# Optimization experiments

Measured on AMD Instinct MI355X. Metric: run time of the kernel, lower is better.

## Reference

```python
import jax, jax.numpy as jnp
import numpy as np

G = 512          # graphs in batch
NPG = 128        # nodes per graph (equal-sized so decoder batches)
TEMP = 0.1       # SimilarityDecoder temperature


def setup_inputs() -> dict:
    key = jax.random.key(0)
    ks = jax.random.split(key, 10)
    N, D, K, H, T = G * NPG, 512, 1024, 128, 10
    return {
        "x": jax.random.normal(ks[0], (N, D), jnp.float32),
        "batch": jnp.repeat(jnp.arange(G, dtype=jnp.int64), NPG),
        "codebook_input": jax.random.normal(ks[1], (K, D), jnp.float32),
        "fc1_w": jax.random.normal(ks[2], (H, D), jnp.float32) * (1.0 / np.sqrt(D)),
        "fc1_b": jax.random.normal(ks[3], (H,), jnp.float32) * 0.01,
        "fc2_w": jax.random.normal(ks[4], (D, H), jnp.float32) * (1.0 / np.sqrt(H)),
        "fc2_b": jax.random.normal(ks[5], (D,), jnp.float32) * 0.01,
        "causal": jax.random.normal(ks[6], (K, K), jnp.float32),
        "cls_w": jax.random.normal(ks[7], (T, D), jnp.float32) * (1.0 / np.sqrt(D)),
        "cls_b": jax.random.normal(ks[8], (T,), jnp.float32) * 0.01,
    }


def _segment_mean(v, batch, num_segments):
    s = jax.ops.segment_sum(v, batch, num_segments=num_segments)
    cnt = jax.ops.segment_sum(jnp.ones((v.shape[0], 1), v.dtype), batch, num_segments=num_segments)
    return s / jnp.maximum(cnt, 1.0)


def _batched_adj(z):
    # SimilarityDecoder: per-graph sigmoid(norm_z @ norm_z.T / temp); graphs equal-sized -> [G, n, n]
    zg = z.reshape(G, NPG, -1)
    zn = zg / jnp.maximum(jnp.linalg.norm(zg, axis=-1, keepdims=True), 1e-12)
    return jax.nn.sigmoid(jnp.einsum("gnd,gmd->gnm", zn, zn) / TEMP)


def reference(x, batch, codebook_input, fc1_w, fc1_b, fc2_w, fc2_b, causal, cls_w, cls_b):
    K = causal.shape[0]
    I = jnp.eye(K, dtype=x.dtype)

    # ---- VectorQuantizer ----
    h = jax.nn.sigmoid(codebook_input @ fc1_w.T + fc1_b)
    codebook_transformed = h @ fc2_w.T + fc2_b                 # [K, D]
    causal_effect = causal * (1.0 - I) + I                     # off-diag causal + identity
    cs = jax.nn.sigmoid(codebook_transformed)
    causal_diag = causal * I
    causal_cb = causal_effect @ (causal_diag @ cs)             # [K, D]
    counter_matrix = causal * (1.0 - I)                        # DegreeLayer assumed: off-diagonal mask
    counter_cb = causal_effect @ (counter_matrix @ cs)         # [K, D]

    # ---- ClassLayer ----
    pooled_x = _segment_mean(x, batch, G)                      # [G, D]
    # squared euclidean distances x vs causal_cb -> argmin codebook index
    d2 = (jnp.sum(x * x, 1, keepdims=True)
          - 2.0 * (x @ causal_cb.T)
          + jnp.sum(causal_cb * causal_cb, 1))                 # [N, K]
    idx = jnp.argmin(d2, axis=1)                               # [N]
    causal_nodes = x + causal_cb[idx]
    counter_nodes = counter_cb[idx]
    z_nodes = codebook_transformed[idx]                        # [N, D]
    pooled_causal = _segment_mean(causal_nodes, batch, G)
    pooled_counter = _segment_mean(counter_nodes, batch, G)
    causal_pre = pooled_causal @ cls_w.T + cls_b
    counter_pre = pooled_counter @ cls_w.T + cls_b
    y_pre = pooled_x @ jax.lax.stop_gradient(cls_w).T + jax.lax.stop_gradient(cls_b)

    # ---- SimilarityDecoder ----
    A_ori = _batched_adj(x)                                    # [G, n, n]
    A_rec = _batched_adj(z_nodes)

    return (causal_pre, counter_pre, y_pre, A_ori, A_rec,
            z_nodes, x, causal_diag, counter_matrix, pooled_causal, pooled_x)
```

## Files before the change

kernel.cpp:

```cpp
#include <hip/hip_runtime.h>
#include <math.h>

#define NG   512
#define NPG  128
#define NN   65536
#define DD   512
#define KK   1024
#define HH   128
#define TT   10

#define RES_TAU 1.0f
#define RES_CAP 65536

typedef __attribute__((ext_vector_type(8))) short short8;
typedef __attribute__((ext_vector_type(4))) float float4v;

static const long OFF_CPRE = 0;
static const long OFF_KPRE = 5120;
static const long OFF_YPRE = 10240;
static const long OFF_AORI = 15360;
static const long OFF_AREC = OFF_AORI + 8388608L;
static const long OFF_Z    = OFF_AREC + 8388608L;
static const long OFF_X    = OFF_Z + 33554432L;
static const long OFF_CD   = OFF_X + 33554432L;
static const long OFF_CM   = OFF_CD + 1048576L;
static const long OFF_PC   = OFF_CM + 1048576L;
static const long OFF_PX   = OFF_PC + 262144L;

__device__ __forceinline__ float sigm_fast(float v) { return 1.0f / (1.0f + __expf(-v)); }
__device__ __forceinline__ float sigm_acc (float v) { return 1.0f / (1.0f + expf(-v)); }

__global__ void k_diagmask(const float* __restrict__ causal,
                           float* __restrict__ cd, float* __restrict__ cm,
                           float* __restrict__ dv) {
  int i = blockIdx.x * 256 + threadIdx.x;
  int r = i >> 10, c = i & 1023;
  float v = causal[i];
  bool diag = (r == c);
  cd[i] = diag ? v : 0.0f;
  cm[i] = diag ? 0.0f : v;
  if (diag) dv[r] = v;
}

__global__ void k_fc1(const float* __restrict__ cbi, const float* __restrict__ w,
                      const float* __restrict__ b, float* __restrict__ h) {
  int i = blockIdx.x * 256 + threadIdx.x;
  int k = i >> 7, j = i & 127;
  const float4* xr = (const float4*)(cbi + (long)k * DD);
  const float4* wr = (const float4*)(w + (long)j * DD);
  float s = b[j];
  for (int d = 0; d < DD / 4; d++) {
    float4 a = xr[d], bb = wr[d];
    s += a.x * bb.x + a.y * bb.y + a.z * bb.z + a.w * bb.w;
  }
  h[i] = sigm_acc(s);
}

__global__ void k_fc2(const float* __restrict__ h, const float* __restrict__ w,
                      const float* __restrict__ b, float* __restrict__ ct,
                      float* __restrict__ cs) {
  int i = blockIdx.x * 256 + threadIdx.x;
  int k = i >> 9, d = i & 511;
  const float4* hr = (const float4*)(h + (long)k * HH);
  const float4* wr = (const float4*)(w + (long)d * HH);
  float s = b[d];
  for (int j = 0; j < HH / 4; j++) {
    float4 a = hr[j], bb = wr[j];
    s += a.x * bb.x + a.y * bb.y + a.z * bb.z + a.w * bb.w;
  }
  ct[i] = s;
  cs[i] = sigm_acc(s);
}

template <int AM, int BM>
__launch_bounds__(256)
__global__ void gemm64(const float* __restrict__ A, const float* __restrict__ B,
                       const float* __restrict__ dscale, float* __restrict__ C,
                       int M, int Nc, int Kr) {
  __shared__ __align__(16) float as[32][68];
  __shared__ __align__(16) float bs[32][68];
  int tid = threadIdx.x;
  int tx = tid & 15, ty = tid >> 4;
  int m0 = blockIdx.y * 64, n0 = blockIdx.x * 64;
  float acc[4][4] = {};
  for (int kt = 0; kt < Kr; kt += 32) {
    for (int s = tid; s < 512; s += 256) {
      int m = s >> 3, c4 = (s & 7) << 2;
      int gr = m0 + m, gc = kt + c4;
      float4 v = *(const float4*)&A[(long)gr * Kr + gc];
      float vv[4] = {v.x, v.y, v.z, v.w};
      if (AM == 1) {
#pragma unroll
        for (int q = 0; q < 4; q++) if (gc + q == gr) vv[q] = 1.0f;
      } else if (AM == 2) {
#pragma unroll
        for (int q = 0; q < 4; q++) if (gc + q == gr) vv[q] = 0.0f;
      }
      as[c4 + 0][m] = vv[0]; as[c4 + 1][m] = vv[1];
      as[c4 + 2][m] = vv[2]; as[c4 + 3][m] = vv[3];
    }
    for (int s = tid; s < 512; s += 256) {
      int r = s >> 4, c4 = (s & 15) << 2;
      float4 v = *(const float4*)&B[(long)(kt + r) * Nc + n0 + c4];
      if (BM == 1) {
        float sc = dscale[kt + r];
        v.x *= sc; v.y *= sc; v.z *= sc; v.w *= sc;
      }
      *(float4*)&bs[r][c4] = v;
    }
    __syncthreads();
#pragma unroll
    for (int r = 0; r < 32; r++) {
      float4 a4 = *(const float4*)&as[r][ty * 4];
      float4 b4 = *(const float4*)&bs[r][tx * 4];
      float av[4] = {a4.x, a4.y, a4.z, a4.w};
      float bv[4] = {b4.x, b4.y, b4.z, b4.w};
#pragma unroll
      for (int i = 0; i < 4; i++)
#pragma unroll
        for (int j = 0; j < 4; j++) acc[i][j] += av[i] * bv[j];
    }
    __syncthreads();
  }
#pragma unroll
  for (int i = 0; i < 4; i++) {
    float4 v = make_float4(acc[i][0], acc[i][1], acc[i][2], acc[i][3]);
    *(float4*)&C[(long)(m0 + ty * 4 + i) * Nc + n0 + tx * 4] = v;
  }
}

__global__ void k_cnorm(const float* __restrict__ ccb, float* __restrict__ cn2,
                        int* __restrict__ rc) {
  if (blockIdx.x == 0 && threadIdx.x == 0) *rc = 0;
  int row = blockIdx.x * 4 + (threadIdx.x >> 6);
  int lane = threadIdx.x & 63;
  const float* r = ccb + (long)row * DD;
  float s = 0.0f;
  for (int q = 0; q < DD; q += 64) { float v = r[lane + q]; s += v * v; }
  for (int off = 32; off > 0; off >>= 1) s += __shfl_down(s, off);
  if (lane == 0) cn2[row] = s;
}

__device__ __forceinline__ ushort bf16_rne(float f, float* back) {
  unsigned int b = __float_as_uint(f);
  unsigned int r = b + 0x7fffu + ((b >> 16) & 1u);
  ushort h = (ushort)(r >> 16);
  *back = __uint_as_float(((unsigned int)h) << 16);
  return h;
}

__global__ void k_split(const float4* __restrict__ src, ushort* __restrict__ hi,
                        ushort* __restrict__ lo, long n4) {
  long i = (long)blockIdx.x * 256 + threadIdx.x;
  if (i >= n4) return;
  float4 v = src[i];
  float vv[4] = {v.x, v.y, v.z, v.w};
  ushort h[4], l[4];
#pragma unroll
  for (int q = 0; q < 4; q++) {
    float back;
    h[q] = bf16_rne(vv[q], &back);
    float rem = vv[q] - back;
    float dummy;
    l[q] = bf16_rne(rem, &dummy);
  }
  ((ushort4*)hi)[i] = make_ushort4(h[0], h[1], h[2], h[3]);
  ((ushort4*)lo)[i] = make_ushort4(l[0], l[1], l[2], l[3]);
}

__launch_bounds__(256)
__global__ void k_argmin_mfma(const ushort* __restrict__ xh, const ushort* __restrict__ xl,
                              const ushort* __restrict__ ch, const ushort* __restrict__ cl,
                              const float* __restrict__ cn2, int* __restrict__ idxg,
                              int* __restrict__ rc, int* __restrict__ rlist) {
  __shared__ __align__(16) ushort xsh[128 * 40];
  __shared__ __align__(16) ushort xsl[128 * 40];
  __shared__ __align__(16) ushort csh[128 * 40];
  __shared__ __align__(16) ushort csl[128 * 40];
  __shared__ float cn2s[KK];
  __shared__ float mm1[2][128], mm2[2][128];
  __shared__ int   mid[2][128];

  int tid = threadIdx.x;
  for (int s = tid; s < KK; s += 256) cn2s[s] = cn2[s];
  long n0 = (long)blockIdx.x * 128;
  int lane = tid & 63, wave = tid >> 6;
  int wy = wave >> 1, wx = wave & 1;
  int col = lane & 15, quad = lane >> 4;

  float m1[16], m2[16]; int id1[16];
#pragma unroll
  for (int s = 0; s < 16; s++) { m1[s] = 3.4e38f; m2[s] = 3.4e38f; id1[s] = 0; }

  const float4v vzero = {0.0f, 0.0f, 0.0f, 0.0f};
  float4v acc[4][4];

  for (int cb = 0; cb < 8; cb++) {
#pragma unroll
    for (int i = 0; i < 4; i++)
#pragma unroll
      for (int j = 0; j < 4; j++) acc[i][j] = vzero;
    long cbase = (long)cb * 128;
    for (int dt = 0; dt < DD; dt += 32) {
      __syncthreads();
      for (int s = tid; s < 512; s += 256) {
        int row = s >> 2, part = s & 3;
        int gc = dt + part * 8;
        int lo = row * 40 + part * 8;
        *(uint4*)&xsh[lo] = *(const uint4*)&xh[(n0 + row) * DD + gc];
        *(uint4*)&xsl[lo] = *(const uint4*)&xl[(n0 + row) * DD + gc];
        *(uint4*)&csh[lo] = *(const uint4*)&ch[(cbase + row) * DD + gc];
        *(uint4*)&csl[lo] = *(const uint4*)&cl[(cbase + row) * DD + gc];
      }
      __syncthreads();
      short8 ah[4], al[4];
#pragma unroll
      for (int i = 0; i < 4; i++) {
        int ro = (wy * 64 + i * 16 + col) * 40 + quad * 8;
        ah[i] = *(const short8*)&xsh[ro];
        al[i] = *(const short8*)&xsl[ro];
      }
#pragma unroll
      for (int j = 0; j < 4; j++) {
        int ro = (wx * 64 + j * 16 + col) * 40 + quad * 8;
        short8 bh = *(const short8*)&csh[ro];
        short8 bl = *(const short8*)&csl[ro];
#pragma unroll
        for (int i = 0; i < 4; i++) {
          acc[i][j] = __builtin_amdgcn_mfma_f32_16x16x32_bf16(ah[i], bh, acc[i][j], 0, 0, 0);
          acc[i][j] = __builtin_amdgcn_mfma_f32_16x16x32_bf16(ah[i], bl, acc[i][j], 0, 0, 0);
          acc[i][j] = __builtin_amdgcn_mfma_f32_16x16x32_bf16(al[i], bh, acc[i][j], 0, 0, 0);
        }
      }
    }
#pragma unroll
    for (int j = 0; j < 4; j++) {
      int code = cb * 128 + wx * 64 + j * 16 + col;
      float c2 = cn2s[code];
#pragma unroll
      for (int i = 0; i < 4; i++) {
#pragma unroll
        for (int r = 0; r < 4; r++) {
          float v = fmaf(-2.0f, acc[i][j][r], c2);
          int s = i * 4 + r;
          if (v < m1[s] || (v == m1[s] && code < id1[s])) {
            m2[s] = m1[s]; m1[s] = v; id1[s] = code;
          } else if (v < m2[s]) {
            m2[s] = v;
          }
        }
      }
    }
  }
#pragma unroll
  for (int s = 0; s < 16; s++) {
#pragma unroll
    for (int mask = 1; mask <= 8; mask <<= 1) {
      float om1 = __shfl_xor(m1[s], mask);
      float om2 = __shfl_xor(m2[s], mask);
      int   oid = __shfl_xor(id1[s], mask);
      if (om1 < m1[s] || (om1 == m1[s] && oid < id1[s])) {
        m2[s] = fminf(m1[s], om2); m1[s] = om1; id1[s] = oid;
      } else {
        m2[s] = fminf(m2[s], om1);
      }
    }
  }
  if (col == 0) {
#pragma unroll
    for (int s = 0; s < 16; s++) {
      int i = s >> 2, r = s & 3;
      int nl = wy * 64 + i * 16 + quad * 4 + r;
      mm1[wx][nl] = m1[s]; mm2[wx][nl] = m2[s]; mid[wx][nl] = id1[s];
    }
  }
  __syncthreads();
  if (tid < 128) {
    float a1 = mm1[0][tid], a2 = mm2[0][tid]; int ai = mid[0][tid];
    float b1 = mm1[1][tid], b2 = mm2[1][tid]; int bi = mid[1][tid];
    float f1, f2; int fi;
    if (b1 < a1 || (b1 == a1 && bi < ai)) { f1 = b1; fi = bi; f2 = fminf(a1, b2); }
    else                                  { f1 = a1; fi = ai; f2 = fminf(a2, b1); }
    idxg[n0 + tid] = fi;
    if (f2 - f1 < RES_TAU) {
      int p = atomicAdd(rc, 1);
      if (p < RES_CAP) rlist[p] = (int)(n0 + tid);
    }
  }
}

__global__ void k_rescue(const float* __restrict__ x, const float* __restrict__ ccb,
                         const float* __restrict__ cn2, const int* __restrict__ rc,
                         const int* __restrict__ rlist, int* __restrict__ idxg) {
  __shared__ float xs[DD];
  __shared__ float bv[256]; __shared__ int bi[256];
  int count = *rc; if (count > RES_CAP) count = RES_CAP;
  int tid = threadIdx.x;
  for (int f = blockIdx.x; f < count; f += gridDim.x) {
    int n = rlist[f];
    for (int s = tid; s < DD; s += 256) xs[s] = x[(long)n * DD + s];
    __syncthreads();
    float best = 3.4e38f; int besti = 0;
    for (int c = tid; c < KK; c += 256) {
      const float4* cr = (const float4*)(ccb + (long)c * DD);
      const float4* xr = (const float4*)xs;
      float dot = 0.0f;
      for (int d = 0; d < DD / 4; d++) {
        float4 a = xr[d], b = cr[d];
        dot += a.x * b.x + a.y * b.y + a.z * b.z + a.w * b.w;
      }
      float v = cn2[c] - 2.0f * dot;
      if (v < best || (v == best && c < besti)) { best = v; besti = c; }
    }
    bv[tid] = best; bi[tid] = besti;
    __syncthreads();
    for (int off = 128; off > 0; off >>= 1) {
      if (tid < off) {
        float ov = bv[tid + off]; int oi = bi[tid + off];
        if (ov < bv[tid] || (ov == bv[tid] && oi < bi[tid])) { bv[tid] = ov; bi[tid] = oi; }
      }
      __syncthreads();
    }
    if (tid == 0) idxg[n] = bi[0];
    __syncthreads();
  }
}

__global__ void k_gather(const float4* __restrict__ ct4, const int* __restrict__ idxg,
                         float4* __restrict__ z4) {
  long i = (long)blockIdx.x * 256 + threadIdx.x;
  int n = (int)(i >> 7), c = (int)(i & 127);
  z4[i] = ct4[(long)idxg[n] * 128 + c];
}

__global__ void k_pool(const float* __restrict__ x, const float* __restrict__ ccb,
                       const float* __restrict__ kcb, const int* __restrict__ idxg,
                       float* __restrict__ px, float* __restrict__ pc,
                       float* __restrict__ pk) {
  __shared__ int sidx[NPG];
  int g = blockIdx.x, tid = threadIdx.x;
  if (tid < NPG) sidx[tid] = idxg[g * NPG + tid];
  __syncthreads();
  int d = tid;
  float sx = 0.0f, sc = 0.0f, sk = 0.0f;
  for (int n = 0; n < NPG; n++) {
    sx += x[((long)g * NPG + n) * DD + d];
    long r = (long)sidx[n] * DD + d;
    sc += ccb[r]; sk += kcb[r];
  }
  px[(long)g * DD + d] = sx / 128.0f;
  pc[(long)g * DD + d] = (sx + sc) / 128.0f;
  pk[(long)g * DD + d] = sk / 128.0f;
}

__global__ void k_heads(const float* __restrict__ pc, const float* __restrict__ pk,
                        const float* __restrict__ px, const float* __restrict__ w,
                        const float* __restrict__ b, float* __restrict__ cpre,
                        float* __restrict__ kpre, float* __restrict__ ypre) {
  int g = blockIdx.x, t = threadIdx.x;
  if (t >= 30) return;
  int which = t / 10, tt = t % 10;
  const float* src = (which == 0) ? pc : ((which == 1) ? pk : px);
  const float* sr = src + (long)g * DD;
  const float* wr = w + (long)tt * DD;
  float s = 0.0f;
  for (int d = 0; d < DD; d++) s += sr[d] * wr[d];
  s += b[tt];
  float* dst = (which == 0) ? cpre : ((which == 1) ? kpre : ypre);
  dst[g * TT + tt] = s;
}

__global__ void k_copy(const float4* __restrict__ src, float4* __restrict__ dst) {
  long i = (long)blockIdx.x * 256 + threadIdx.x;
  dst[i] = src[i];
}

__launch_bounds__(256)
__global__ void k_adj(const float* __restrict__ Z, float* __restrict__ Aout) {
  __shared__ float nrm[NPG];
  __shared__ float inv[NPG];
  __shared__ __align__(16) float zs[32][132];
  int tid = threadIdx.x;
  int g = blockIdx.x;
  const float* base = Z + (long)g * NPG * DD;
  if (tid < NPG) nrm[tid] = 0.0f;
  __syncthreads();
  for (int k = 0; k < 64; k++) {
    long i = (long)k * 256 + tid;
    int n = (int)(i >> 7);
    float4 v = ((const float4*)base)[i];
    float s = v.x * v.x + v.y * v.y + v.z * v.z + v.w * v.w;
    for (int off = 32; off > 0; off >>= 1) s += __shfl_down(s, off);
    if ((tid & 63) == 0) atomicAdd(&nrm[n], s);
  }
  __syncthreads();
  if (tid < NPG) inv[tid] = 1.0f / fmaxf(sqrtf(nrm[tid]), 1e-12f);
  __syncthreads();
  float acc[8][8] = {};
  int tx = tid & 15, ty = tid >> 4;
  for (int dt = 0; dt < DD; dt += 32) {
    for (int s = tid; s < 1024; s += 256) {
      int n = s >> 3, c4 = (s & 7) << 2;
      float4 v = *(const float4*)&base[(long)n * DD + dt + c4];
      float iv = inv[n];
      zs[c4 + 0][n] = v.x * iv; zs[c4 + 1][n] = v.y * iv;
      zs[c4 + 2][n] = v.z * iv; zs[c4 + 3][n] = v.w * iv;
    }
    __syncthreads();
#pragma unroll 8
    for (int r = 0; r < 32; r++) {
      float rv[8], cv[8];
      *(float4*)&rv[0] = *(const float4*)&zs[r][ty * 8];
      *(float4*)&rv[4] = *(const float4*)&zs[r][ty * 8 + 4];
      *(float4*)&cv[0] = *(const float4*)&zs[r][tx * 8];
      *(float4*)&cv[4] = *(const float4*)&zs[r][tx * 8 + 4];
#pragma unroll
      for (int i = 0; i < 8; i++)
#pragma unroll
        for (int j = 0; j < 8; j++) acc[i][j] += rv[i] * cv[j];
    }
    __syncthreads();
  }
  float* aout = Aout + (long)g * NPG * NPG;
#pragma unroll
  for (int i = 0; i < 8; i++) {
    int rr = ty * 8 + i;
    float o[8];
#pragma unroll
    for (int j = 0; j < 8; j++) o[j] = sigm_fast(acc[i][j] * 10.0f);
    *(float4*)&aout[(long)rr * NPG + tx * 8]     = make_float4(o[0], o[1], o[2], o[3]);
    *(float4*)&aout[(long)rr * NPG + tx * 8 + 4] = make_float4(o[4], o[5], o[6], o[7]);
  }
}

extern "C" void kernel_launch(void* const* d_in, const int* in_sizes, int n_in,
                              void* d_out, int out_size, void* d_ws, size_t ws_size,
                              hipStream_t stream) {
  const float* x      = (const float*)d_in[0];
  const float* cbi    = (const float*)d_in[2];
  const float* fc1w   = (const float*)d_in[3];
  const float* fc1b   = (const float*)d_in[4];
  const float* fc2w   = (const float*)d_in[5];
  const float* fc2b   = (const float*)d_in[6];
  const float* causal = (const float*)d_in[7];
  const float* clsw   = (const float*)d_in[8];
  const float* clsb   = (const float*)d_in[9];
  float* out = (float*)d_out;

  float* cpre = out + OFF_CPRE;
  float* kpre = out + OFF_KPRE;
  float* ypre = out + OFF_YPRE;

  float* scr  = out + OFF_AORI;
  float* h    = scr;
  float* cs   = scr + 131072L;
  float* tmp2 = scr + 655360L;
  float* ccb  = scr + 1179648L;
  float* kcb  = scr + 1703936L;
  float* cn2  = scr + 2228224L;
  int*   idxg = (int*)(scr + 2229248L);
  float* pk   = scr + 2294784L;
  float* dv   = scr + 2556928L;
  ushort* ch  = (ushort*)(scr + 2557952L);
  ushort* cl  = (ushort*)(scr + 2820096L);
  int*   rc   = (int*)(scr + 3082240L);
  int*   rlist= (int*)(scr + 3082496L);
  float* ct   = out + OFF_AREC;
  ushort* xh  = (ushort*)(out + OFF_X);
  ushort* xl  = (ushort*)(out + OFF_X + 16777216L);

  k_diagmask<<<4096, 256, 0, stream>>>(causal, out + OFF_CD, out + OFF_CM, dv);
  k_fc1<<<512, 256, 0, stream>>>(cbi, fc1w, fc1b, h);
  k_fc2<<<2048, 256, 0, stream>>>(h, fc2w, fc2b, ct, cs);
  gemm64<2, 0><<<dim3(8, 16), 256, 0, stream>>>(causal, cs,   nullptr, tmp2, KK, DD, KK);
  gemm64<1, 1><<<dim3(8, 16), 256, 0, stream>>>(causal, cs,   dv,      ccb,  KK, DD, KK);
  gemm64<1, 0><<<dim3(8, 16), 256, 0, stream>>>(causal, tmp2, nullptr, kcb,  KK, DD, KK);
  k_cnorm<<<256, 256, 0, stream>>>(ccb, cn2, rc);
  k_split<<<32768, 256, 0, stream>>>((const float4*)x, xh, xl, 8388608L);
  k_split<<<512, 256, 0, stream>>>((const float4*)ccb, ch, cl, 131072L);
  k_argmin_mfma<<<512, 256, 0, stream>>>(xh, xl, ch, cl, cn2, idxg, rc, rlist);
  k_rescue<<<128, 256, 0, stream>>>(x, ccb, cn2, rc, rlist, idxg);
  k_gather<<<32768, 256, 0, stream>>>((const float4*)ct, idxg, (float4*)(out + OFF_Z));
  k_pool<<<512, 512, 0, stream>>>(x, ccb, kcb, idxg, out + OFF_PX, out + OFF_PC, pk);
  k_heads<<<512, 64, 0, stream>>>(out + OFF_PC, pk, out + OFF_PX, clsw, clsb, cpre, kpre, ypre);
  k_copy<<<32768, 256, 0, stream>>>((const float4*)x, (float4*)(out + OFF_X));
  k_adj<<<512, 256, 0, stream>>>(out + OFF_Z, out + OFF_AREC);
  k_adj<<<512, 256, 0, stream>>>(x, out + OFF_AORI);
}
```

Measured before the change: 1.819 ms.

## Keep node tile resident in LDS and stream codebook fragments from global

The argmin MFMA kernel now loads a 64-node hi/lo bf16 tile (full D) into LDS once, with an XOR swizzle to avoid bank conflicts. Each of 8 waves then streams its own 64-code slice of the codebook straight from global/L2 into registers, which removes the per-k-step LDS staging and the two barriers per iteration. The grid doubles to 1024 blocks of 512 threads with a cross-wave min-reduction. The trade-off is more global/L2 traffic for codebook fragments and 64KB+ of LDS per block, which limits occupancy.

```diff
diff --git a/kernel.cpp b/kernel.cpp
--- a/kernel.cpp
+++ b/kernel.cpp
@@ -168,24 +168,44 @@
   ((ushort4*)lo)[i] = make_ushort4(l[0], l[1], l[2], l[3]);
 }
 
-__launch_bounds__(256)
+__launch_bounds__(512, 2)
 __global__ void k_argmin_mfma(const ushort* __restrict__ xh, const ushort* __restrict__ xl,
                               const ushort* __restrict__ ch, const ushort* __restrict__ cl,
                               const float* __restrict__ cn2, int* __restrict__ idxg,
                               int* __restrict__ rc, int* __restrict__ rlist) {
-  __shared__ __align__(16) ushort xsh[128 * 40];
-  __shared__ __align__(16) ushort xsl[128 * 40];
-  __shared__ __align__(16) ushort csh[128 * 40];
-  __shared__ __align__(16) ushort csl[128 * 40];
+  __shared__ __align__(16) ushort xsh[64 * 512];
+  __shared__ __align__(16) ushort xsl[64 * 512];
   __shared__ float cn2s[KK];
-  __shared__ float mm1[2][128], mm2[2][128];
-  __shared__ int   mid[2][128];
+  __shared__ float mm1[8][64], mm2[8][64];
+  __shared__ int   mid[8][64];
 
   int tid = threadIdx.x;
-  for (int s = tid; s < KK; s += 256) cn2s[s] = cn2[s];
-  long n0 = (long)blockIdx.x * 128;
+  long n0 = (long)blockIdx.x * 64;
+
+  uint4 tmp[16];
+#pragma unroll
+  for (int r = 0; r < 16; r++) {
+    int g = tid + r * 512;
+    int rid = g >> 6;
+    int node = rid & 63;
+    int gb = (g & 63) << 4;
+    const ushort* src = ((rid < 64) ? xh : xl) + (n0 + node) * (long)DD;
+    tmp[r] = *(const uint4*)((const char*)src + gb);
+  }
+  for (int s = tid; s < KK; s += 512) cn2s[s] = cn2[s];
+#pragma unroll
+  for (int r = 0; r < 16; r++) {
+    int g = tid + r * 512;
+    int rid = g >> 6;
+    int node = rid & 63;
+    int gb = (g & 63) << 4;
+    int db = gb ^ ((node & 7) << 4);
+    ushort* dst = (rid < 64) ? xsh : xsl;
+    *(uint4*)((char*)dst + node * 1024 + db) = tmp[r];
+  }
+  __syncthreads();
+
   int lane = tid & 63, wave = tid >> 6;
-  int wy = wave >> 1, wx = wave & 1;
   int col = lane & 15, quad = lane >> 4;
 
   float m1[16], m2[16]; int id1[16];
@@ -195,47 +215,44 @@
   const float4v vzero = {0.0f, 0.0f, 0.0f, 0.0f};
   float4v acc[4][4];
 
-  for (int cb = 0; cb < 8; cb++) {
+  for (int cc = 0; cc < 2; cc++) {
+    int cb0 = cc * 512 + wave * 64;
 #pragma unroll
     for (int i = 0; i < 4; i++)
 #pragma unroll
       for (int j = 0; j < 4; j++) acc[i][j] = vzero;
-    long cbase = (long)cb * 128;
+
     for (int dt = 0; dt < DD; dt += 32) {
-      __syncthreads();
-      for (int s = tid; s < 512; s += 256) {
-        int row = s >> 2, part = s & 3;
-        int gc = dt + part * 8;
-        int lo = row * 40 + part * 8;
-        *(uint4*)&xsh[lo] = *(const uint4*)&xh[(n0 + row) * DD + gc];
-        *(uint4*)&xsl[lo] = *(const uint4*)&xl[(n0 + row) * DD + gc];
-        *(uint4*)&csh[lo] = *(const uint4*)&ch[(cbase + row) * DD + gc];
-        *(uint4*)&csl[lo] = *(const uint4*)&cl[(cbase + row) * DD + gc];
-      }
-      __syncthreads();
+      short8 bh[4], bl[4];
+#pragma unroll
+      for (int j = 0; j < 4; j++) {
+        long crow = (long)(cb0 + j * 16 + col);
+        const ushort* cph = ch + crow * DD + dt + quad * 8;
+        const ushort* cpl = cl + crow * DD + dt + quad * 8;
+        bh[j] = *(const short8*)cph;
+        bl[j] = *(const short8*)cpl;
+      }
       short8 ah[4], al[4];
 #pragma unroll
       for (int i = 0; i < 4; i++) {
-        int ro = (wy * 64 + i * 16 + col) * 40 + quad * 8;
-        ah[i] = *(const short8*)&xsh[ro];
-        al[i] = *(const short8*)&xsl[ro];
+        int node = i * 16 + col;
+        int db = (dt * 2 + quad * 16) ^ ((node & 7) << 4);
+        ah[i] = *(const short8*)((const char*)xsh + node * 1024 + db);
+        al[i] = *(const short8*)((const char*)xsl + node * 1024 + db);
       }
 #pragma unroll
       for (int j = 0; j < 4; j++) {
-        int ro = (wx * 64 + j * 16 + col) * 40 + quad * 8;
-        short8 bh = *(const short8*)&csh[ro];
-        short8 bl = *(const short8*)&csl[ro];
 #pragma unroll
         for (int i = 0; i < 4; i++) {
-          acc[i][j] = __builtin_amdgcn_mfma_f32_16x16x32_bf16(ah[i], bh, acc[i][j], 0, 0, 0);
-          acc[i][j] = __builtin_amdgcn_mfma_f32_16x16x32_bf16(ah[i], bl, acc[i][j], 0, 0, 0);
-          acc[i][j] = __builtin_amdgcn_mfma_f32_16x16x32_bf16(al[i], bh, acc[i][j], 0, 0, 0);
+          acc[i][j] = __builtin_amdgcn_mfma_f32_16x16x32_bf16(ah[i], bh[j], acc[i][j], 0, 0, 0);
+          acc[i][j] = __builtin_amdgcn_mfma_f32_16x16x32_bf16(ah[i], bl[j], acc[i][j], 0, 0, 0);
+          acc[i][j] = __builtin_amdgcn_mfma_f32_16x16x32_bf16(al[i], bh[j], acc[i][j], 0, 0, 0);
         }
       }
     }
 #pragma unroll
     for (int j = 0; j < 4; j++) {
-      int code = cb * 128 + wx * 64 + j * 16 + col;
+      int code = cb0 + j * 16 + col;
       float c2 = cn2s[code];
 #pragma unroll
       for (int i = 0; i < 4; i++) {
@@ -270,17 +287,22 @@
 #pragma unroll
     for (int s = 0; s < 16; s++) {
       int i = s >> 2, r = s & 3;
-      int nl = wy * 64 + i * 16 + quad * 4 + r;
-      mm1[wx][nl] = m1[s]; mm2[wx][nl] = m2[s]; mid[wx][nl] = id1[s];
+      int nl = i * 16 + quad * 4 + r;
+      mm1[wave][nl] = m1[s]; mm2[wave][nl] = m2[s]; mid[wave][nl] = id1[s];
     }
   }
   __syncthreads();
-  if (tid < 128) {
-    float a1 = mm1[0][tid], a2 = mm2[0][tid]; int ai = mid[0][tid];
-    float b1 = mm1[1][tid], b2 = mm2[1][tid]; int bi = mid[1][tid];
-    float f1, f2; int fi;
-    if (b1 < a1 || (b1 == a1 && bi < ai)) { f1 = b1; fi = bi; f2 = fminf(a1, b2); }
-    else                                  { f1 = a1; fi = ai; f2 = fminf(a2, b1); }
+  if (tid < 64) {
+    float f1 = mm1[0][tid], f2 = mm2[0][tid]; int fi = mid[0][tid];
+#pragma unroll
+    for (int w = 1; w < 8; w++) {
+      float b1 = mm1[w][tid], b2 = mm2[w][tid]; int bi = mid[w][tid];
+      if (b1 < f1 || (b1 == f1 && bi < fi)) {
+        f2 = fminf(f1, b2); f1 = b1; fi = bi;
+      } else {
+        f2 = fminf(f2, b1);
+      }
+    }
     idxg[n0 + tid] = fi;
     if (f2 - f1 < RES_TAU) {
       int p = atomicAdd(rc, 1);
@@ -478,7 +500,7 @@
   k_cnorm<<<256, 256, 0, stream>>>(ccb, cn2, rc);
   k_split<<<32768, 256, 0, stream>>>((const float4*)x, xh, xl, 8388608L);
   k_split<<<512, 256, 0, stream>>>((const float4*)ccb, ch, cl, 131072L);
-  k_argmin_mfma<<<512, 256, 0, stream>>>(xh, xl, ch, cl, cn2, idxg, rc, rlist);
+  k_argmin_mfma<<<1024, 512, 0, stream>>>(xh, xl, ch, cl, cn2, idxg, rc, rlist);
   k_rescue<<<128, 256, 0, stream>>>(x, ccb, cn2, rc, rlist, idxg);
   k_gather<<<32768, 256, 0, stream>>>((const float4*)ct, idxg, (float4*)(out + OFF_Z));
   k_pool<<<512, 512, 0, stream>>>(x, ccb, kcb, idxg, out + OFF_PX, out + OFF_PC, pk);
```

New measurement: 1.767 ms. -2.9%, faster.
